# Kernel optimization log

Hardware: AMD Instinct MI355X
Metric: run time of the kernel (lower is better)

Reference implementation:

```python
import jax, jax.numpy as jnp
import numpy as np

N_NODES = 500_000
N_EDGES = 8_000_000
BN_EPS = 1e-5


def _graph_embed(src, dst, n, W_init, b_init, Wg, bg, Wt1, g1, b1, Wt2, g2, b2, Wd, bd):
    # init_graph: input is all-ones [n, 12] -> Linear(12->4); every row identical
    x_row = W_init.sum(0) + b_init                      # [4]
    h_row = jax.nn.sigmoid(x_row @ Wg + bg)             # node gating -> [7]
    h = jnp.broadcast_to(h_row, (n, h_row.shape[0]))    # [n, 7]

    # symmetric normalization, DGL TAGConv style
    deg = jnp.zeros((n,), jnp.float32).at[dst].add(1.0)
    norm = jnp.clip(deg, 1.0) ** -0.5                   # [n]

    def prop(x):  # x: [n, d] -> normalized adjacency propagation
        x = x * norm[:, None]
        agg = jnp.zeros_like(x).at[dst].add(x[src])
        return agg * norm[:, None]

    def tagconv(x, W):  # K=2: concat [h, Ah, A^2h] then linear (no bias)
        f1 = prop(x)
        f2 = prop(f1)
        return jnp.concatenate([x, f1, f2], axis=1) @ W

    def bn_relu(x, gamma, beta):  # BatchNorm1d training-mode (batch stats)
        m = x.mean(0)
        v = x.var(0)
        return jax.nn.relu((x - m) / jnp.sqrt(v + BN_EPS) * gamma + beta)

    h = bn_relu(tagconv(h, Wt1), g1, b1)
    h = bn_relu(tagconv(h, Wt2), g2, b2)
    h = h @ Wd + bd                                     # [n, 11]
    return h.mean(0)                                    # [11] graph embedding


def setup_inputs() -> dict:
    key = jax.random.key(0)
    ks = jax.random.split(key, 32)
    n, e = N_NODES, N_EDGES
    d = {
        "src1": jax.random.randint(ks[0], (e,), 0, n, dtype=jnp.int32),
        "dst1": jax.random.randint(ks[1], (e,), 0, n, dtype=jnp.int32),
        "src2": jax.random.randint(ks[2], (e,), 0, n, dtype=jnp.int32),
        "dst2": jax.random.randint(ks[3], (e,), 0, n, dtype=jnp.int32),
        "n_nodes": n,
    }
    def w(k, shape):
        return jax.random.normal(k, shape, jnp.float32) * 0.1
    # GraphEmbed params (node_emb=4, size_graph_emb=11, layers=(7,7), TAGConv K=2)
    d["W_init"] = w(ks[4], (12, 4)); d["b_init"] = w(ks[5], (4,))
    d["Wg"] = w(ks[6], (4, 7));      d["bg"] = w(ks[7], (7,))
    d["Wt1"] = w(ks[8], (21, 7))
    d["bn1_g"] = jnp.ones((7,), jnp.float32); d["bn1_b"] = jnp.zeros((7,), jnp.float32)
    d["Wt2"] = w(ks[9], (21, 7))
    d["bn2_g"] = jnp.ones((7,), jnp.float32); d["bn2_b"] = jnp.zeros((7,), jnp.float32)
    d["Wd"] = w(ks[10], (7, 11));    d["bd"] = w(ks[11], (11,))
    # GraphSimilarity params (embedding_space=11, layers=(7,7,7), 12 properties)
    d["Ws0"] = w(ks[12], (22, 7));   d["bs0"] = w(ks[13], (7,))
    d["Ws1"] = w(ks[14], (7, 7));    d["bs1"] = w(ks[15], (7,))
    d["Ws2"] = w(ks[16], (7, 7));    d["bs2"] = w(ks[17], (7,))
    d["Ws3"] = w(ks[18], (7, 7));    d["bs3"] = w(ks[19], (7,))
    d["Wsim"] = w(ks[20], (7, 12));  d["bsim"] = w(ks[21], (12,))
    return d


def reference(src1, dst1, src2, dst2, n_nodes,
              W_init, b_init, Wg, bg, Wt1, bn1_g, bn1_b, Wt2, bn2_g, bn2_b, Wd, bd,
              Ws0, bs0, Ws1, bs1, Ws2, bs2, Ws3, bs3, Wsim, bsim):
    emb = lambda s, t: _graph_embed(s, t, n_nodes, W_init, b_init, Wg, bg,
                                    Wt1, bn1_g, bn1_b, Wt2, bn2_g, bn2_b, Wd, bd)
    hg1 = emb(src1, dst1)
    hg2 = emb(src2, dst2)
    h = jnp.concatenate([hg1, hg2])[None, :]            # [1, 22]
    h = h @ Ws0 + bs0
    for W, b in ((Ws1, bs1), (Ws2, bs2), (Ws3, bs3)):
        h = jax.nn.relu(h @ W + b)
    logits = h @ Wsim + bsim                            # [1, 12]
    # sigmoid on locality logit and sigmoid on remaining diffs == elementwise sigmoid
    return jax.nn.sigmoid(logits)
```

## Files before the change

### kernel.cpp

```cpp
#include <hip/hip_runtime.h>
#include <hip/hip_bf16.h>
#include <math.h>

#define NNODES 500000
#define BN_EPS 1e-5f
#define BKT 512
#define NBKT ((NNODES + BKT - 1) / BKT)
#define EPB 16384

__device__ __forceinline__ int atomAddI(int* p, int v) {
    return __hip_atomic_fetch_add(p, v, __ATOMIC_RELAXED, __HIP_MEMORY_SCOPE_AGENT);
}
__device__ __forceinline__ void atomAddD(double* p, double v) {
    __hip_atomic_fetch_add(p, v, __ATOMIC_RELAXED, __HIP_MEMORY_SCOPE_AGENT);
}
__device__ __forceinline__ void ldsAddF(float* p, float v) {
    __hip_atomic_fetch_add(p, v, __ATOMIC_RELAXED, __HIP_MEMORY_SCOPE_WORKGROUP);
}

template<int CNT>
__device__ __forceinline__ void blk_reduce_atomic(double (&vals)[CNT], double* dst) {
    __shared__ double sh[CNT][4];
    int lane = threadIdx.x & 63, wid = threadIdx.x >> 6;
#pragma unroll
    for (int k = 0; k < CNT; ++k) {
        double v = vals[k];
#pragma unroll
        for (int o = 32; o; o >>= 1) v += __shfl_down(v, o);
        if (lane == 0) sh[k][wid] = v;
    }
    __syncthreads();
    if ((int)threadIdx.x < CNT) {
        double v = sh[threadIdx.x][0] + sh[threadIdx.x][1] + sh[threadIdx.x][2] + sh[threadIdx.x][3];
        atomAddD(dst + threadIdx.x, v);
    }
}

__global__ void k_t0(const float* __restrict__ Wi, const float* __restrict__ bi,
                     const float* __restrict__ Wg, const float* __restrict__ bg,
                     const float* __restrict__ Wt1, float* __restrict__ fs) {
    if (threadIdx.x || blockIdx.x) return;
    float xr[4];
    for (int j = 0; j < 4; ++j) {
        float s = bi[j];
        for (int k = 0; k < 12; ++k) s += Wi[k * 4 + j];
        xr[j] = s;
    }
    float hr[7];
    for (int j = 0; j < 7; ++j) {
        float s = bg[j];
        for (int k = 0; k < 4; ++k) s += xr[k] * Wg[k * 7 + j];
        hr[j] = 1.f / (1.f + expf(-s));
        fs[j] = hr[j];
    }
    for (int j = 0; j < 7; ++j) {
        float s0 = 0.f, s1 = 0.f, s2 = 0.f;
        for (int k = 0; k < 7; ++k) {
            s0 += hr[k] * Wt1[k * 7 + j];
            s1 += hr[k] * Wt1[(7 + k) * 7 + j];
            s2 += hr[k] * Wt1[(14 + k) * 7 + j];
        }
        fs[7 + j] = s0; fs[14 + j] = s1; fs[21 + j] = s2;
    }
}

__global__ void __launch_bounds__(256) k_bhist(const int* __restrict__ dst, int* __restrict__ gcnt, int E) {
    __shared__ int h[NBKT];
    for (int i = threadIdx.x; i < NBKT; i += 256) h[i] = 0;
    __syncthreads();
    int base = blockIdx.x * EPB;
#pragma unroll
    for (int k = 0; k < EPB / 1024; ++k) {
        int i4 = base + (k * 256 + threadIdx.x) * 4;
        if (i4 + 3 < E) {
            int4 d = *reinterpret_cast<const int4*>(dst + i4);
            atomicAdd(&h[d.x >> 9], 1); atomicAdd(&h[d.y >> 9], 1);
            atomicAdd(&h[d.z >> 9], 1); atomicAdd(&h[d.w >> 9], 1);
        } else {
            for (int i = i4; i < E && i < i4 + 4; ++i) atomicAdd(&h[dst[i] >> 9], 1);
        }
    }
    __syncthreads();
    for (int i = threadIdx.x; i < NBKT; i += 256)
        if (h[i]) atomAddI(gcnt + i, h[i]);
}

__global__ void __launch_bounds__(1024) k_bscan(const int* __restrict__ gcnt,
                                                int* __restrict__ bb, int* __restrict__ gcur) {
    __shared__ int sh[1024];
    int t = threadIdx.x;
    int v = (t < NBKT) ? gcnt[t] : 0;
    sh[t] = v; __syncthreads();
    for (int o = 1; o < 1024; o <<= 1) {
        int x = (t >= o) ? sh[t - o] : 0;
        __syncthreads();
        sh[t] += x;
        __syncthreads();
    }
    if (t < NBKT) { int ex = sh[t] - v; bb[t] = ex; gcur[t] = ex; }
    if (t == 0) bb[NBKT] = sh[1023];
}

__global__ void __launch_bounds__(256) k_bscat(const int* __restrict__ src, const int* __restrict__ dst,
                                               int* __restrict__ gcur, unsigned int* __restrict__ pairs, int E) {
    __shared__ int h[NBKT];
    for (int i = threadIdx.x; i < NBKT; i += 256) h[i] = 0;
    __syncthreads();
    int base = blockIdx.x * EPB;
#pragma unroll
    for (int k = 0; k < EPB / 1024; ++k) {
        int i4 = base + (k * 256 + threadIdx.x) * 4;
        if (i4 + 3 < E) {
            int4 d = *reinterpret_cast<const int4*>(dst + i4);
            atomicAdd(&h[d.x >> 9], 1); atomicAdd(&h[d.y >> 9], 1);
            atomicAdd(&h[d.z >> 9], 1); atomicAdd(&h[d.w >> 9], 1);
        } else {
            for (int i = i4; i < E && i < i4 + 4; ++i) atomicAdd(&h[dst[i] >> 9], 1);
        }
    }
    __syncthreads();
    for (int i = threadIdx.x; i < NBKT; i += 256) {
        int c = h[i];
        h[i] = c ? atomAddI(gcur + i, c) : 0;
    }
    __syncthreads();
#pragma unroll
    for (int k = 0; k < EPB / 1024; ++k) {
        int i4 = base + (k * 256 + threadIdx.x) * 4;
        if (i4 + 3 < E) {
            int4 s = *reinterpret_cast<const int4*>(src + i4);
            int4 d = *reinterpret_cast<const int4*>(dst + i4);
            int se[4] = {s.x, s.y, s.z, s.w};
            int de[4] = {d.x, d.y, d.z, d.w};
#pragma unroll
            for (int e = 0; e < 4; ++e) {
                int b = de[e] >> 9;
                int pos = atomicAdd(&h[b], 1);
                pairs[pos] = ((unsigned int)(de[e] & 511) << 19) | (unsigned int)se[e];
            }
        } else {
            for (int i = i4; i < E && i < i4 + 4; ++i) {
                int b = dst[i] >> 9;
                int pos = atomicAdd(&h[b], 1);
                pairs[pos] = ((unsigned int)(dst[i] & 511) << 19) | (unsigned int)src[i];
            }
        }
    }
}

__global__ void __launch_bounds__(256) k_deg(const unsigned int* __restrict__ pairs, const int* __restrict__ bb,
                                             float* __restrict__ nrm, float* __restrict__ sdeg, int n) {
    __shared__ int deg[BKT];
    int b = blockIdx.x, t = threadIdx.x;
    deg[t] = 0; deg[t + 256] = 0;
    __syncthreads();
    int lo = bb[b], hi = bb[b + 1];
    for (int k = lo + t; k < hi; k += 256) atomicAdd(&deg[pairs[k] >> 19], 1);
    __syncthreads();
#pragma unroll
    for (int j = 0; j < 2; ++j) {
        int dl = t + j * 256, node = b * BKT + dl;
        if (node < n) {
            float sd = sqrtf((float)(deg[dl] > 0 ? deg[dl] : 1));
            sdeg[node] = sd;
            nrm[node] = 1.f / sd;
        }
    }
}

__global__ void __launch_bounds__(256) k_s1(const unsigned int* __restrict__ pairs, const int* __restrict__ bb,
                                            const float* __restrict__ nrm, float* __restrict__ s1,
                                            float* __restrict__ s1n, int n) {
    __shared__ float acc[BKT];
    int b = blockIdx.x, t = threadIdx.x;
    acc[t] = 0.f; acc[t + 256] = 0.f;
    __syncthreads();
    int lo = bb[b], hi = bb[b + 1];
    for (int k = lo + t; k < hi; k += 256) {
        unsigned int v = pairs[k];
        ldsAddF(&acc[v >> 19], nrm[v & 0x7FFFF]);
    }
    __syncthreads();
#pragma unroll
    for (int j = 0; j < 2; ++j) {
        int dl = t + j * 256, node = b * BKT + dl;
        if (node < n) {
            float nn = nrm[node], v1 = acc[dl] * nn;
            s1[node] = v1; s1n[node] = v1 * nn;
        }
    }
}

__global__ void __launch_bounds__(256) k_s2(const unsigned int* __restrict__ pairs, const int* __restrict__ bb,
                                            const float* __restrict__ nrm, const float* __restrict__ s1,
                                            const float* __restrict__ s1n, float* __restrict__ s2,
                                            double* __restrict__ ds, int n) {
    __shared__ float acc[BKT];
    int b = blockIdx.x, t = threadIdx.x;
    acc[t] = 0.f; acc[t + 256] = 0.f;
    __syncthreads();
    int lo = bb[b], hi = bb[b + 1];
    for (int k = lo + t; k < hi; k += 256) {
        unsigned int v = pairs[k];
        ldsAddF(&acc[v >> 19], s1n[v & 0x7FFFF]);
    }
    __syncthreads();
    double m[5] = {0, 0, 0, 0, 0};
#pragma unroll
    for (int j = 0; j < 2; ++j) {
        int dl = t + j * 256, node = b * BKT + dl;
        if (node < n) {
            float nn = nrm[node], v2 = acc[dl] * nn;
            s2[node] = v2;
            float v1 = s1[node];
            m[0] += v1; m[1] += v2;
            m[2] += (double)v1 * (double)v1;
            m[3] += (double)v2 * (double)v2;
            m[4] += (double)v1 * (double)v2;
        }
    }
    blk_reduce_atomic<5>(m, ds);
}

__global__ void k_t1(const double* __restrict__ ds, const float* __restrict__ fs,
                     const float* __restrict__ g1, const float* __restrict__ b1, float* __restrict__ fsg) {
    if (threadIdx.x || blockIdx.x) return;
    const double inv_n = 1.0 / (double)NNODES;
    float mu1 = (float)(ds[0] * inv_n), mu2 = (float)(ds[1] * inv_n);
    float V11 = (float)(ds[2] * inv_n) - mu1 * mu1;
    float V22 = (float)(ds[3] * inv_n) - mu2 * mu2;
    float V12 = (float)(ds[4] * inv_n) - mu1 * mu2;
    for (int j = 0; j < 7; ++j) {
        float a1 = fs[14 + j], a2 = fs[21 + j];
        float var = a1 * a1 * V11 + a2 * a2 * V22 + 2.f * a1 * a2 * V12;
        float ig = (1.f / sqrtf(var + BN_EPS)) * g1[j];
        fsg[j]      = b1[j] - (mu1 * a1 + mu2 * a2) * ig;
        fsg[7 + j]  = a1 * ig;
        fsg[14 + j] = a2 * ig;
    }
}

__global__ void __launch_bounds__(256) k_h1n(const float* __restrict__ s1, const float* __restrict__ s2,
                                             const float* __restrict__ nrm, const float* __restrict__ fsg,
                                             float* __restrict__ h1n, int n) {
    int i = blockIdx.x * blockDim.x + threadIdx.x;
    if (i >= n) return;
    float S1 = s1[i], S2 = s2[i], Nn = nrm[i];
    float o[8];
#pragma unroll
    for (int j = 0; j < 7; ++j)
        o[j] = fmaxf(fsg[j] + S1 * fsg[7 + j] + S2 * fsg[14 + j], 0.f) * Nn;
    o[7] = 0.f;
    float4* q = reinterpret_cast<float4*>(h1n + (size_t)i * 8);
    q[0] = make_float4(o[0], o[1], o[2], o[3]);
    q[1] = make_float4(o[4], o[5], o[6], o[7]);
}

__global__ void __launch_bounds__(256) k_f1(const unsigned int* __restrict__ pairs, const int* __restrict__ bb,
                                            const float* __restrict__ nrm, const float* __restrict__ h1n,
                                            float* __restrict__ f1n, int n) {
    __shared__ float a[7][BKT];
    int b = blockIdx.x, t = threadIdx.x;
#pragma unroll
    for (int j = 0; j < 7; ++j) { a[j][t] = 0.f; a[j][t + 256] = 0.f; }
    __syncthreads();
    int lo = bb[b], hi = bb[b + 1];
    for (int k = lo + t; k < hi; k += 256) {
        unsigned int v = pairs[k];
        int s = v & 0x7FFFF, dl = v >> 19;
        const float4* p = reinterpret_cast<const float4*>(h1n + (size_t)s * 8);
        float4 x = p[0], y = p[1];
        ldsAddF(&a[0][dl], x.x); ldsAddF(&a[1][dl], x.y); ldsAddF(&a[2][dl], x.z);
        ldsAddF(&a[3][dl], x.w); ldsAddF(&a[4][dl], y.x); ldsAddF(&a[5][dl], y.y);
        ldsAddF(&a[6][dl], y.z);
    }
    __syncthreads();
#pragma unroll
    for (int j = 0; j < 2; ++j) {
        int dl = t + j * 256, node = b * BKT + dl;
        if (node < n) {
            float nn = nrm[node], sc = nn * nn;
            float4* q = reinterpret_cast<float4*>(f1n + (size_t)node * 8);
            q[0] = make_float4(a[0][dl] * sc, a[1][dl] * sc, a[2][dl] * sc, a[3][dl] * sc);
            q[1] = make_float4(a[4][dl] * sc, a[5][dl] * sc, a[6][dl] * sc, 0.f);
        }
    }
}

__global__ void __launch_bounds__(256) k_x2f(const unsigned int* __restrict__ pairs, const int* __restrict__ bb,
                                             const float* __restrict__ nrm, const float* __restrict__ sdeg,
                                             const float* __restrict__ s1, const float* __restrict__ s2,
                                             const float* __restrict__ fsg, const float* __restrict__ f1n,
                                             const float* __restrict__ Wt2, float* __restrict__ x2o,
                                             double* __restrict__ ds, int n) {
    __shared__ float a[7][BKT];
    __shared__ float w[147];
    int b = blockIdx.x, t = threadIdx.x;
    for (int k = t; k < 147; k += 256) w[k] = Wt2[k];
    float dc[21];
#pragma unroll
    for (int j = 0; j < 21; ++j) dc[j] = fsg[j];
#pragma unroll
    for (int j = 0; j < 7; ++j) { a[j][t] = 0.f; a[j][t + 256] = 0.f; }
    __syncthreads();
    int lo = bb[b], hi = bb[b + 1];
    for (int k = lo + t; k < hi; k += 256) {
        unsigned int v = pairs[k];
        int s = v & 0x7FFFF, dl = v >> 19;
        const float4* p = reinterpret_cast<const float4*>(f1n + (size_t)s * 8);
        float4 x = p[0], y = p[1];
        ldsAddF(&a[0][dl], x.x); ldsAddF(&a[1][dl], x.y); ldsAddF(&a[2][dl], x.z);
        ldsAddF(&a[3][dl], x.w); ldsAddF(&a[4][dl], y.x); ldsAddF(&a[5][dl], y.y);
        ldsAddF(&a[6][dl], y.z);
    }
    __syncthreads();
    double sx[7] = {0, 0, 0, 0, 0, 0, 0}, sq[7] = {0, 0, 0, 0, 0, 0, 0};
#pragma unroll
    for (int jj = 0; jj < 2; ++jj) {
        int dl = t + jj * 256, node = b * BKT + dl;
        if (node < n) {
            float S1 = s1[node], S2 = s2[node], Nn = nrm[node], rn = sdeg[node];
            float h1[7];
#pragma unroll
            for (int k = 0; k < 7; ++k) h1[k] = fmaxf(dc[k] + S1 * dc[7 + k] + S2 * dc[14 + k], 0.f);
            const float4* pf = reinterpret_cast<const float4*>(f1n + (size_t)node * 8);
            float4 fa = pf[0], fb = pf[1];
            float f1p[7] = {fa.x * rn, fa.y * rn, fa.z * rn, fa.w * rn, fb.x * rn, fb.y * rn, fb.z * rn};
            float f2p[7];
#pragma unroll
            for (int k = 0; k < 7; ++k) f2p[k] = a[k][dl] * Nn;
            float x2[8];
#pragma unroll
            for (int j = 0; j < 7; ++j) {
                float s = 0.f;
#pragma unroll
                for (int k = 0; k < 7; ++k)
                    s += h1[k] * w[k * 7 + j] + f1p[k] * w[(7 + k) * 7 + j] + f2p[k] * w[(14 + k) * 7 + j];
                x2[j] = s;
                sx[j] += s; sq[j] += (double)s * (double)s;
            }
            x2[7] = 0.f;
            float4* q = reinterpret_cast<float4*>(x2o + (size_t)node * 8);
            q[0] = make_float4(x2[0], x2[1], x2[2], x2[3]);
            q[1] = make_float4(x2[4], x2[5], x2[6], x2[7]);
        }
    }
    double acc[14];
#pragma unroll
    for (int j = 0; j < 7; ++j) { acc[j] = sx[j]; acc[7 + j] = sq[j]; }
    blk_reduce_atomic<14>(acc, ds + 5);
}

__global__ void k_t2(const double* __restrict__ ds, const float* __restrict__ g2,
                     const float* __restrict__ b2, float* __restrict__ fsg) {
    if (threadIdx.x || blockIdx.x) return;
    const double inv_n = 1.0 / (double)NNODES;
    for (int j = 0; j < 7; ++j) {
        float m = (float)(ds[5 + j] * inv_n);
        float v = (float)(ds[12 + j] * inv_n) - m * m;
        float ig = (1.f / sqrtf(v + BN_EPS)) * g2[j];
        fsg[21 + j] = b2[j] - m * ig;
        fsg[28 + j] = ig;
    }
}

__global__ void __launch_bounds__(256) k_h2sum(const float* __restrict__ x2o, const float* __restrict__ fsg,
                                               double* __restrict__ ds, int n) {
    float c0[7], c1[7];
#pragma unroll
    for (int j = 0; j < 7; ++j) { c0[j] = fsg[21 + j]; c1[j] = fsg[28 + j]; }
    double acc[7] = {0, 0, 0, 0, 0, 0, 0};
    for (int i = blockIdx.x * blockDim.x + threadIdx.x; i < n; i += gridDim.x * blockDim.x) {
        const float4* p = reinterpret_cast<const float4*>(x2o + (size_t)i * 8);
        float4 a = p[0], b = p[1];
        float x[7] = {a.x, a.y, a.z, a.w, b.x, b.y, b.z};
#pragma unroll
        for (int j = 0; j < 7; ++j) acc[j] += (double)fmaxf(x[j] * c1[j] + c0[j], 0.f);
    }
    blk_reduce_atomic<7>(acc, ds + 19);
}

__global__ void k_final(const double* __restrict__ ds, const float* __restrict__ Wd, const float* __restrict__ bd,
                        const float* __restrict__ Ws0, const float* __restrict__ bs0,
                        const float* __restrict__ Ws1, const float* __restrict__ bs1,
                        const float* __restrict__ Ws2, const float* __restrict__ bs2,
                        const float* __restrict__ Ws3, const float* __restrict__ bs3,
                        const float* __restrict__ Wsim, const float* __restrict__ bsim,
                        float* __restrict__ out) {
    if (threadIdx.x || blockIdx.x) return;
    const double inv_n = 1.0 / (double)NNODES;
    float v[22];
    for (int g = 0; g < 2; ++g) {
        float hm[7];
        for (int j = 0; j < 7; ++j) hm[j] = (float)(ds[g * 26 + 19 + j] * inv_n);
        for (int r = 0; r < 11; ++r) {
            float s = bd[r];
            for (int j = 0; j < 7; ++j) s += hm[j] * Wd[j * 11 + r];
            v[g * 11 + r] = s;
        }
    }
    float h[7], h2[7];
    for (int j = 0; j < 7; ++j) {
        float s = bs0[j];
        for (int k = 0; k < 22; ++k) s += v[k] * Ws0[k * 7 + j];
        h[j] = s;
    }
    const float* Ws[3] = {Ws1, Ws2, Ws3};
    const float* bs[3] = {bs1, bs2, bs3};
    for (int l = 0; l < 3; ++l) {
        for (int j = 0; j < 7; ++j) {
            float s = bs[l][j];
            for (int k = 0; k < 7; ++k) s += h[k] * Ws[l][k * 7 + j];
            h2[j] = fmaxf(s, 0.f);
        }
        for (int j = 0; j < 7; ++j) h[j] = h2[j];
    }
    for (int r = 0; r < 12; ++r) {
        float s = bsim[r];
        for (int j = 0; j < 7; ++j) s += h[j] * Wsim[j * 12 + r];
        out[r] = 1.f / (1.f + expf(-s));
    }
}

extern "C" void kernel_launch(void* const* d_in, const int* in_sizes, int n_in,
                              void* d_out, int out_size, void* d_ws, size_t ws_size,
                              hipStream_t stream) {
    const int E = in_sizes[0];
    const int n = NNODES;
    const int* src1 = (const int*)d_in[0];
    const int* dst1 = (const int*)d_in[1];
    const int* src2 = (const int*)d_in[2];
    const int* dst2 = (const int*)d_in[3];
    const float* W_init = (const float*)d_in[5];
    const float* b_init = (const float*)d_in[6];
    const float* Wg  = (const float*)d_in[7];
    const float* bg  = (const float*)d_in[8];
    const float* Wt1 = (const float*)d_in[9];
    const float* g1  = (const float*)d_in[10];
    const float* b1  = (const float*)d_in[11];
    const float* Wt2 = (const float*)d_in[12];
    const float* g2  = (const float*)d_in[13];
    const float* b2  = (const float*)d_in[14];
    const float* Wd  = (const float*)d_in[15];
    const float* bd  = (const float*)d_in[16];
    const float* Ws0 = (const float*)d_in[17];
    const float* bs0 = (const float*)d_in[18];
    const float* Ws1 = (const float*)d_in[19];
    const float* bs1 = (const float*)d_in[20];
    const float* Ws2 = (const float*)d_in[21];
    const float* bs2 = (const float*)d_in[22];
    const float* Ws3 = (const float*)d_in[23];
    const float* bs3 = (const float*)d_in[24];
    const float* Wsim = (const float*)d_in[25];
    const float* bsim = (const float*)d_in[26];

    float* F     = (float*)d_ws;
    float* norm  = F;
    float* sdeg  = F + (size_t)n;
    float* s1    = F + 2 * (size_t)n;
    float* s1n   = F + 3 * (size_t)n;
    float* s2    = F + 4 * (size_t)n;
    float* h1n   = F + 5 * (size_t)n;
    float* f1n   = F + 13 * (size_t)n;
    int*   gcnt  = (int*)(F + 21 * (size_t)n);
    int*   bb    = gcnt + NBKT;
    int*   gcur  = bb + NBKT + 1;
    unsigned int* pairs = (unsigned int*)(gcur + NBKT);
    float* fscal = (float*)(pairs + E);
    size_t dso = ((size_t)(fscal + 128 - F) + 1) & ~(size_t)1;
    double* dscal = (double*)(F + dso);

    const int EB  = (E + EPB - 1) / EPB;
    const int nbk = (n + 255) / 256;
    const int rbk = 1024;

    hipMemsetAsync(dscal, 0, 52 * sizeof(double), stream);
    k_t0<<<1, 1, 0, stream>>>(W_init, b_init, Wg, bg, Wt1, fscal);

    for (int g = 0; g < 2; ++g) {
        const int* src = g ? src2 : src1;
        const int* dst = g ? dst2 : dst1;
        float* fsg  = fscal + 28 + g * 35;
        double* dsg = dscal + g * 26;

        hipMemsetAsync(gcnt, 0, NBKT * sizeof(int), stream);
        k_bhist<<<EB, 256, 0, stream>>>(dst, gcnt, E);
        k_bscan<<<1, 1024, 0, stream>>>(gcnt, bb, gcur);
        k_bscat<<<EB, 256, 0, stream>>>(src, dst, gcur, pairs, E);

        k_deg<<<NBKT, 256, 0, stream>>>(pairs, bb, norm, sdeg, n);
        k_s1 <<<NBKT, 256, 0, stream>>>(pairs, bb, norm, s1, s1n, n);
        k_s2 <<<NBKT, 256, 0, stream>>>(pairs, bb, norm, s1, s1n, s2, dsg, n);
        k_t1<<<1, 1, 0, stream>>>(dsg, fscal, g1, b1, fsg);
        k_h1n<<<nbk, 256, 0, stream>>>(s1, s2, norm, fsg, h1n, n);
        k_f1 <<<NBKT, 256, 0, stream>>>(pairs, bb, norm, h1n, f1n, n);
        k_x2f<<<NBKT, 256, 0, stream>>>(pairs, bb, norm, sdeg, s1, s2, fsg, f1n, Wt2, h1n, dsg, n);
        k_t2<<<1, 1, 0, stream>>>(dsg, g2, b2, fsg);
        k_h2sum<<<rbk, 256, 0, stream>>>(h1n, fsg, dsg, n);
    }
    k_final<<<1, 1, 0, stream>>>(dscal, Wd, bd, Ws0, bs0, Ws1, bs1, Ws2, bs2, Ws3, bs3,
                                 Wsim, bsim, (float*)d_out);
}
```

Baseline: 2.053 ms.

## Fuse layer-1 activation into gather, pack node scalars, store f1 in fp16

Removes the separate k_h1n pass: k_f1 now rebuilds the layer-1 ReLU features on the fly from a packed per-node float4 (s1, s2, norm, sqrt-degree) instead of gathering a 32-byte h1n row. The f1 intermediate is stored as fp16 in 16-byte rows, which halves gather traffic in k_x2f. Bucket kernels move to 512 threads (one per node), and the edge loops are unrolled by two to keep more loads in flight. The cost is extra ALU work per edge in k_f1, a little fp16 precision loss on f1, and a new workspace layout.

```diff
diff --git a/kernel.cpp b/kernel.cpp
--- a/kernel.cpp
+++ b/kernel.cpp
@@ -1,5 +1,6 @@
 #include <hip/hip_runtime.h>
 #include <hip/hip_bf16.h>
+#include <hip/hip_fp16.h>
 #include <math.h>
 
 #define NNODES 500000
@@ -20,7 +21,7 @@
 
 template<int CNT>
 __device__ __forceinline__ void blk_reduce_atomic(double (&vals)[CNT], double* dst) {
-    __shared__ double sh[CNT][4];
+    __shared__ double sh[CNT][8];
     int lane = threadIdx.x & 63, wid = threadIdx.x >> 6;
 #pragma unroll
     for (int k = 0; k < CNT; ++k) {
@@ -31,7 +32,9 @@
     }
     __syncthreads();
     if ((int)threadIdx.x < CNT) {
-        double v = sh[threadIdx.x][0] + sh[threadIdx.x][1] + sh[threadIdx.x][2] + sh[threadIdx.x][3];
+        double v = 0.0;
+#pragma unroll
+        for (int w = 0; w < 8; ++w) v += sh[threadIdx.x][w];
         atomAddD(dst + threadIdx.x, v);
     }
 }
@@ -148,76 +151,83 @@
     }
 }
 
-__global__ void __launch_bounds__(256) k_deg(const unsigned int* __restrict__ pairs, const int* __restrict__ bb,
-                                             float* __restrict__ nrm, float* __restrict__ sdeg, int n) {
+__global__ void __launch_bounds__(512) k_deg(const unsigned int* __restrict__ pairs, const int* __restrict__ bb,
+                                             float* __restrict__ nrm, float* __restrict__ sc4, int n) {
     __shared__ int deg[BKT];
     int b = blockIdx.x, t = threadIdx.x;
-    deg[t] = 0; deg[t + 256] = 0;
+    deg[t] = 0;
     __syncthreads();
     int lo = bb[b], hi = bb[b + 1];
-    for (int k = lo + t; k < hi; k += 256) atomicAdd(&deg[pairs[k] >> 19], 1);
-    __syncthreads();
-#pragma unroll
-    for (int j = 0; j < 2; ++j) {
-        int dl = t + j * 256, node = b * BKT + dl;
-        if (node < n) {
-            float sd = sqrtf((float)(deg[dl] > 0 ? deg[dl] : 1));
-            sdeg[node] = sd;
-            nrm[node] = 1.f / sd;
-        }
-    }
-}
-
-__global__ void __launch_bounds__(256) k_s1(const unsigned int* __restrict__ pairs, const int* __restrict__ bb,
+    int k = lo + t;
+    for (; k + BKT < hi; k += 2 * BKT) {
+        unsigned int v1 = pairs[k], v2 = pairs[k + BKT];
+        atomicAdd(&deg[v1 >> 19], 1);
+        atomicAdd(&deg[v2 >> 19], 1);
+    }
+    if (k < hi) atomicAdd(&deg[pairs[k] >> 19], 1);
+    __syncthreads();
+    int node = b * BKT + t;
+    if (node < n) {
+        float sd = sqrtf((float)(deg[t] > 0 ? deg[t] : 1));
+        float nn = 1.f / sd;
+        nrm[node] = nn;
+        reinterpret_cast<float4*>(sc4)[node] = make_float4(0.f, 0.f, nn, sd);
+    }
+}
+
+__global__ void __launch_bounds__(512) k_s1(const unsigned int* __restrict__ pairs, const int* __restrict__ bb,
                                             const float* __restrict__ nrm, float* __restrict__ s1,
-                                            float* __restrict__ s1n, int n) {
+                                            float* __restrict__ s1n, float* __restrict__ sc4, int n) {
     __shared__ float acc[BKT];
     int b = blockIdx.x, t = threadIdx.x;
-    acc[t] = 0.f; acc[t + 256] = 0.f;
+    acc[t] = 0.f;
     __syncthreads();
     int lo = bb[b], hi = bb[b + 1];
-    for (int k = lo + t; k < hi; k += 256) {
-        unsigned int v = pairs[k];
-        ldsAddF(&acc[v >> 19], nrm[v & 0x7FFFF]);
-    }
-    __syncthreads();
-#pragma unroll
-    for (int j = 0; j < 2; ++j) {
-        int dl = t + j * 256, node = b * BKT + dl;
-        if (node < n) {
-            float nn = nrm[node], v1 = acc[dl] * nn;
-            s1[node] = v1; s1n[node] = v1 * nn;
-        }
-    }
-}
-
-__global__ void __launch_bounds__(256) k_s2(const unsigned int* __restrict__ pairs, const int* __restrict__ bb,
+    int k = lo + t;
+    for (; k + BKT < hi; k += 2 * BKT) {
+        unsigned int v1 = pairs[k], v2 = pairs[k + BKT];
+        float g1 = nrm[v1 & 0x7FFFF], g2 = nrm[v2 & 0x7FFFF];
+        ldsAddF(&acc[v1 >> 19], g1);
+        ldsAddF(&acc[v2 >> 19], g2);
+    }
+    if (k < hi) { unsigned int v = pairs[k]; ldsAddF(&acc[v >> 19], nrm[v & 0x7FFFF]); }
+    __syncthreads();
+    int node = b * BKT + t;
+    if (node < n) {
+        float nn = nrm[node], v1 = acc[t] * nn;
+        s1[node] = v1; s1n[node] = v1 * nn;
+        sc4[(size_t)node * 4 + 0] = v1;
+    }
+}
+
+__global__ void __launch_bounds__(512) k_s2(const unsigned int* __restrict__ pairs, const int* __restrict__ bb,
                                             const float* __restrict__ nrm, const float* __restrict__ s1,
-                                            const float* __restrict__ s1n, float* __restrict__ s2,
+                                            const float* __restrict__ s1n, float* __restrict__ sc4,
                                             double* __restrict__ ds, int n) {
     __shared__ float acc[BKT];
     int b = blockIdx.x, t = threadIdx.x;
-    acc[t] = 0.f; acc[t + 256] = 0.f;
+    acc[t] = 0.f;
     __syncthreads();
     int lo = bb[b], hi = bb[b + 1];
-    for (int k = lo + t; k < hi; k += 256) {
-        unsigned int v = pairs[k];
-        ldsAddF(&acc[v >> 19], s1n[v & 0x7FFFF]);
-    }
+    int k = lo + t;
+    for (; k + BKT < hi; k += 2 * BKT) {
+        unsigned int v1 = pairs[k], v2 = pairs[k + BKT];
+        float g1 = s1n[v1 & 0x7FFFF], g2 = s1n[v2 & 0x7FFFF];
+        ldsAddF(&acc[v1 >> 19], g1);
+        ldsAddF(&acc[v2 >> 19], g2);
+    }
+    if (k < hi) { unsigned int v = pairs[k]; ldsAddF(&acc[v >> 19], s1n[v & 0x7FFFF]); }
     __syncthreads();
     double m[5] = {0, 0, 0, 0, 0};
-#pragma unroll
-    for (int j = 0; j < 2; ++j) {
-        int dl = t + j * 256, node = b * BKT + dl;
-        if (node < n) {
-            float nn = nrm[node], v2 = acc[dl] * nn;
-            s2[node] = v2;
-            float v1 = s1[node];
-            m[0] += v1; m[1] += v2;
-            m[2] += (double)v1 * (double)v1;
-            m[3] += (double)v2 * (double)v2;
-            m[4] += (double)v1 * (double)v2;
-        }
+    int node = b * BKT + t;
+    if (node < n) {
+        float nn = nrm[node], v2 = acc[t] * nn;
+        sc4[(size_t)node * 4 + 1] = v2;
+        float v1 = s1[node];
+        m[0] += v1; m[1] += v2;
+        m[2] += (double)v1 * (double)v1;
+        m[3] += (double)v2 * (double)v2;
+        m[4] += (double)v1 * (double)v2;
     }
     blk_reduce_atomic<5>(m, ds);
 }
@@ -240,110 +250,138 @@
     }
 }
 
-__global__ void __launch_bounds__(256) k_h1n(const float* __restrict__ s1, const float* __restrict__ s2,
-                                             const float* __restrict__ nrm, const float* __restrict__ fsg,
-                                             float* __restrict__ h1n, int n) {
-    int i = blockIdx.x * blockDim.x + threadIdx.x;
-    if (i >= n) return;
-    float S1 = s1[i], S2 = s2[i], Nn = nrm[i];
-    float o[8];
-#pragma unroll
-    for (int j = 0; j < 7; ++j)
-        o[j] = fmaxf(fsg[j] + S1 * fsg[7 + j] + S2 * fsg[14 + j], 0.f) * Nn;
-    o[7] = 0.f;
-    float4* q = reinterpret_cast<float4*>(h1n + (size_t)i * 8);
-    q[0] = make_float4(o[0], o[1], o[2], o[3]);
-    q[1] = make_float4(o[4], o[5], o[6], o[7]);
-}
-
-__global__ void __launch_bounds__(256) k_f1(const unsigned int* __restrict__ pairs, const int* __restrict__ bb,
-                                            const float* __restrict__ nrm, const float* __restrict__ h1n,
-                                            float* __restrict__ f1n, int n) {
+__global__ void __launch_bounds__(512) k_f1(const unsigned int* __restrict__ pairs, const int* __restrict__ bb,
+                                            const float* __restrict__ nrm, const float* __restrict__ sc4,
+                                            const float* __restrict__ fsg, float* __restrict__ f1nh, int n) {
     __shared__ float a[7][BKT];
     int b = blockIdx.x, t = threadIdx.x;
-#pragma unroll
-    for (int j = 0; j < 7; ++j) { a[j][t] = 0.f; a[j][t + 256] = 0.f; }
+    float dc[21];
+#pragma unroll
+    for (int j = 0; j < 21; ++j) dc[j] = fsg[j];
+#pragma unroll
+    for (int j = 0; j < 7; ++j) a[j][t] = 0.f;
     __syncthreads();
     int lo = bb[b], hi = bb[b + 1];
-    for (int k = lo + t; k < hi; k += 256) {
+    int k = lo + t;
+    for (; k + BKT < hi; k += 2 * BKT) {
+        unsigned int v1 = pairs[k], v2 = pairs[k + BKT];
+        float4 r1 = reinterpret_cast<const float4*>(sc4)[v1 & 0x7FFFF];
+        float4 r2 = reinterpret_cast<const float4*>(sc4)[v2 & 0x7FFFF];
+        int d1 = v1 >> 19, d2 = v2 >> 19;
+#pragma unroll
+        for (int j = 0; j < 7; ++j) {
+            float h = fmaxf(dc[j] + r1.x * dc[7 + j] + r1.y * dc[14 + j], 0.f) * r1.z;
+            ldsAddF(&a[j][d1], h);
+        }
+#pragma unroll
+        for (int j = 0; j < 7; ++j) {
+            float h = fmaxf(dc[j] + r2.x * dc[7 + j] + r2.y * dc[14 + j], 0.f) * r2.z;
+            ldsAddF(&a[j][d2], h);
+        }
+    }
+    if (k < hi) {
         unsigned int v = pairs[k];
-        int s = v & 0x7FFFF, dl = v >> 19;
-        const float4* p = reinterpret_cast<const float4*>(h1n + (size_t)s * 8);
-        float4 x = p[0], y = p[1];
-        ldsAddF(&a[0][dl], x.x); ldsAddF(&a[1][dl], x.y); ldsAddF(&a[2][dl], x.z);
-        ldsAddF(&a[3][dl], x.w); ldsAddF(&a[4][dl], y.x); ldsAddF(&a[5][dl], y.y);
-        ldsAddF(&a[6][dl], y.z);
-    }
-    __syncthreads();
-#pragma unroll
-    for (int j = 0; j < 2; ++j) {
-        int dl = t + j * 256, node = b * BKT + dl;
-        if (node < n) {
-            float nn = nrm[node], sc = nn * nn;
-            float4* q = reinterpret_cast<float4*>(f1n + (size_t)node * 8);
-            q[0] = make_float4(a[0][dl] * sc, a[1][dl] * sc, a[2][dl] * sc, a[3][dl] * sc);
-            q[1] = make_float4(a[4][dl] * sc, a[5][dl] * sc, a[6][dl] * sc, 0.f);
-        }
-    }
-}
-
-__global__ void __launch_bounds__(256) k_x2f(const unsigned int* __restrict__ pairs, const int* __restrict__ bb,
-                                             const float* __restrict__ nrm, const float* __restrict__ sdeg,
-                                             const float* __restrict__ s1, const float* __restrict__ s2,
-                                             const float* __restrict__ fsg, const float* __restrict__ f1n,
-                                             const float* __restrict__ Wt2, float* __restrict__ x2o,
-                                             double* __restrict__ ds, int n) {
+        float4 r = reinterpret_cast<const float4*>(sc4)[v & 0x7FFFF];
+        int dl = v >> 19;
+#pragma unroll
+        for (int j = 0; j < 7; ++j) {
+            float h = fmaxf(dc[j] + r.x * dc[7 + j] + r.y * dc[14 + j], 0.f) * r.z;
+            ldsAddF(&a[j][dl], h);
+        }
+    }
+    __syncthreads();
+    int node = b * BKT + t;
+    if (node < n) {
+        float nn = nrm[node], sc = nn * nn;
+        __half2 hh[4];
+        hh[0] = __floats2half2_rn(a[0][t] * sc, a[1][t] * sc);
+        hh[1] = __floats2half2_rn(a[2][t] * sc, a[3][t] * sc);
+        hh[2] = __floats2half2_rn(a[4][t] * sc, a[5][t] * sc);
+        hh[3] = __floats2half2_rn(a[6][t] * sc, 0.f);
+        reinterpret_cast<float4*>(f1nh)[node] = *reinterpret_cast<float4*>(hh);
+    }
+}
+
+__global__ void __launch_bounds__(512) k_x2f(const unsigned int* __restrict__ pairs, const int* __restrict__ bb,
+                                             const float* __restrict__ sc4, const float* __restrict__ fsg,
+                                             const float* __restrict__ f1nh, const float* __restrict__ Wt2,
+                                             float* __restrict__ x2o, double* __restrict__ ds, int n) {
     __shared__ float a[7][BKT];
     __shared__ float w[147];
     int b = blockIdx.x, t = threadIdx.x;
-    for (int k = t; k < 147; k += 256) w[k] = Wt2[k];
+    for (int k = t; k < 147; k += 512) w[k] = Wt2[k];
     float dc[21];
 #pragma unroll
     for (int j = 0; j < 21; ++j) dc[j] = fsg[j];
 #pragma unroll
-    for (int j = 0; j < 7; ++j) { a[j][t] = 0.f; a[j][t + 256] = 0.f; }
+    for (int j = 0; j < 7; ++j) a[j][t] = 0.f;
     __syncthreads();
     int lo = bb[b], hi = bb[b + 1];
-    for (int k = lo + t; k < hi; k += 256) {
+    int k = lo + t;
+    for (; k + BKT < hi; k += 2 * BKT) {
+        unsigned int v1 = pairs[k], v2 = pairs[k + BKT];
+        float4 raw1 = reinterpret_cast<const float4*>(f1nh)[v1 & 0x7FFFF];
+        float4 raw2 = reinterpret_cast<const float4*>(f1nh)[v2 & 0x7FFFF];
+        int d1 = v1 >> 19, d2 = v2 >> 19;
+        {
+            const __half2* hp = reinterpret_cast<const __half2*>(&raw1);
+            float2 q0 = __half22float2(hp[0]), q1 = __half22float2(hp[1]);
+            float2 q2 = __half22float2(hp[2]), q3 = __half22float2(hp[3]);
+            ldsAddF(&a[0][d1], q0.x); ldsAddF(&a[1][d1], q0.y); ldsAddF(&a[2][d1], q1.x);
+            ldsAddF(&a[3][d1], q1.y); ldsAddF(&a[4][d1], q2.x); ldsAddF(&a[5][d1], q2.y);
+            ldsAddF(&a[6][d1], q3.x);
+        }
+        {
+            const __half2* hp = reinterpret_cast<const __half2*>(&raw2);
+            float2 q0 = __half22float2(hp[0]), q1 = __half22float2(hp[1]);
+            float2 q2 = __half22float2(hp[2]), q3 = __half22float2(hp[3]);
+            ldsAddF(&a[0][d2], q0.x); ldsAddF(&a[1][d2], q0.y); ldsAddF(&a[2][d2], q1.x);
+            ldsAddF(&a[3][d2], q1.y); ldsAddF(&a[4][d2], q2.x); ldsAddF(&a[5][d2], q2.y);
+            ldsAddF(&a[6][d2], q3.x);
+        }
+    }
+    if (k < hi) {
         unsigned int v = pairs[k];
-        int s = v & 0x7FFFF, dl = v >> 19;
-        const float4* p = reinterpret_cast<const float4*>(f1n + (size_t)s * 8);
-        float4 x = p[0], y = p[1];
-        ldsAddF(&a[0][dl], x.x); ldsAddF(&a[1][dl], x.y); ldsAddF(&a[2][dl], x.z);
-        ldsAddF(&a[3][dl], x.w); ldsAddF(&a[4][dl], y.x); ldsAddF(&a[5][dl], y.y);
-        ldsAddF(&a[6][dl], y.z);
+        float4 raw = reinterpret_cast<const float4*>(f1nh)[v & 0x7FFFF];
+        int dl = v >> 19;
+        const __half2* hp = reinterpret_cast<const __half2*>(&raw);
+        float2 q0 = __half22float2(hp[0]), q1 = __half22float2(hp[1]);
+        float2 q2 = __half22float2(hp[2]), q3 = __half22float2(hp[3]);
+        ldsAddF(&a[0][dl], q0.x); ldsAddF(&a[1][dl], q0.y); ldsAddF(&a[2][dl], q1.x);
+        ldsAddF(&a[3][dl], q1.y); ldsAddF(&a[4][dl], q2.x); ldsAddF(&a[5][dl], q2.y);
+        ldsAddF(&a[6][dl], q3.x);
     }
     __syncthreads();
     double sx[7] = {0, 0, 0, 0, 0, 0, 0}, sq[7] = {0, 0, 0, 0, 0, 0, 0};
-#pragma unroll
-    for (int jj = 0; jj < 2; ++jj) {
-        int dl = t + jj * 256, node = b * BKT + dl;
-        if (node < n) {
-            float S1 = s1[node], S2 = s2[node], Nn = nrm[node], rn = sdeg[node];
-            float h1[7];
-#pragma unroll
-            for (int k = 0; k < 7; ++k) h1[k] = fmaxf(dc[k] + S1 * dc[7 + k] + S2 * dc[14 + k], 0.f);
-            const float4* pf = reinterpret_cast<const float4*>(f1n + (size_t)node * 8);
-            float4 fa = pf[0], fb = pf[1];
-            float f1p[7] = {fa.x * rn, fa.y * rn, fa.z * rn, fa.w * rn, fb.x * rn, fb.y * rn, fb.z * rn};
-            float f2p[7];
-#pragma unroll
-            for (int k = 0; k < 7; ++k) f2p[k] = a[k][dl] * Nn;
-            float x2[8];
-#pragma unroll
-            for (int j = 0; j < 7; ++j) {
-                float s = 0.f;
-#pragma unroll
-                for (int k = 0; k < 7; ++k)
-                    s += h1[k] * w[k * 7 + j] + f1p[k] * w[(7 + k) * 7 + j] + f2p[k] * w[(14 + k) * 7 + j];
-                x2[j] = s;
-                sx[j] += s; sq[j] += (double)s * (double)s;
-            }
-            x2[7] = 0.f;
-            float4* q = reinterpret_cast<float4*>(x2o + (size_t)node * 8);
-            q[0] = make_float4(x2[0], x2[1], x2[2], x2[3]);
-            q[1] = make_float4(x2[4], x2[5], x2[6], x2[7]);
-        }
+    int node = b * BKT + t;
+    if (node < n) {
+        float4 s = reinterpret_cast<const float4*>(sc4)[node];
+        float S1 = s.x, S2 = s.y, Nn = s.z, rn = s.w;
+        float h1[7];
+#pragma unroll
+        for (int kk = 0; kk < 7; ++kk) h1[kk] = fmaxf(dc[kk] + S1 * dc[7 + kk] + S2 * dc[14 + kk], 0.f);
+        float4 raw = reinterpret_cast<const float4*>(f1nh)[node];
+        const __half2* hp = reinterpret_cast<const __half2*>(&raw);
+        float2 q0 = __half22float2(hp[0]), q1 = __half22float2(hp[1]);
+        float2 q2 = __half22float2(hp[2]), q3 = __half22float2(hp[3]);
+        float f1p[7] = {q0.x * rn, q0.y * rn, q1.x * rn, q1.y * rn, q2.x * rn, q2.y * rn, q3.x * rn};
+        float f2p[7];
+#pragma unroll
+        for (int kk = 0; kk < 7; ++kk) f2p[kk] = a[kk][t] * Nn;
+        float x2[8];
+#pragma unroll
+        for (int j = 0; j < 7; ++j) {
+            float sacc = 0.f;
+#pragma unroll
+            for (int kk = 0; kk < 7; ++kk)
+                sacc += h1[kk] * w[kk * 7 + j] + f1p[kk] * w[(7 + kk) * 7 + j] + f2p[kk] * w[(14 + kk) * 7 + j];
+            x2[j] = sacc;
+            sx[j] += sacc; sq[j] += (double)sacc * (double)sacc;
+        }
+        x2[7] = 0.f;
+        float4* q = reinterpret_cast<float4*>(x2o + (size_t)node * 8);
+        q[0] = make_float4(x2[0], x2[1], x2[2], x2[3]);
+        q[1] = make_float4(x2[4], x2[5], x2[6], x2[7]);
     }
     double acc[14];
 #pragma unroll
@@ -364,7 +402,7 @@
     }
 }
 
-__global__ void __launch_bounds__(256) k_h2sum(const float* __restrict__ x2o, const float* __restrict__ fsg,
+__global__ void __launch_bounds__(512) k_h2sum(const float* __restrict__ x2o, const float* __restrict__ fsg,
                                                double* __restrict__ ds, int n) {
     float c0[7], c1[7];
 #pragma unroll
@@ -454,25 +492,21 @@
     const float* Wsim = (const float*)d_in[25];
     const float* bsim = (const float*)d_in[26];
 
-    float* F     = (float*)d_ws;
-    float* norm  = F;
-    float* sdeg  = F + (size_t)n;
-    float* s1    = F + 2 * (size_t)n;
-    float* s1n   = F + 3 * (size_t)n;
-    float* s2    = F + 4 * (size_t)n;
-    float* h1n   = F + 5 * (size_t)n;
-    float* f1n   = F + 13 * (size_t)n;
-    int*   gcnt  = (int*)(F + 21 * (size_t)n);
-    int*   bb    = gcnt + NBKT;
-    int*   gcur  = bb + NBKT + 1;
+    double* dscal = (double*)d_ws;
+    float* fscal  = (float*)(dscal + 52);
+    float* F      = (float*)((char*)d_ws + 1024);
+    float* nrm  = F;
+    float* s1   = F + (size_t)n;
+    float* s1n  = F + 2 * (size_t)n;
+    float* sc4  = F + 3 * (size_t)n;
+    float* f1nh = F + 7 * (size_t)n;
+    float* x2o  = F + 11 * (size_t)n;
+    int*   gcnt = (int*)(F + 19 * (size_t)n);
+    int*   bb   = gcnt + NBKT;
+    int*   gcur = bb + NBKT + 1;
     unsigned int* pairs = (unsigned int*)(gcur + NBKT);
-    float* fscal = (float*)(pairs + E);
-    size_t dso = ((size_t)(fscal + 128 - F) + 1) & ~(size_t)1;
-    double* dscal = (double*)(F + dso);
-
-    const int EB  = (E + EPB - 1) / EPB;
-    const int nbk = (n + 255) / 256;
-    const int rbk = 1024;
+
+    const int EB = (E + EPB - 1) / EPB;
 
     hipMemsetAsync(dscal, 0, 52 * sizeof(double), stream);
     k_t0<<<1, 1, 0, stream>>>(W_init, b_init, Wg, bg, Wt1, fscal);
@@ -488,15 +522,14 @@
         k_bscan<<<1, 1024, 0, stream>>>(gcnt, bb, gcur);
         k_bscat<<<EB, 256, 0, stream>>>(src, dst, gcur, pairs, E);
 
-        k_deg<<<NBKT, 256, 0, stream>>>(pairs, bb, norm, sdeg, n);
-        k_s1 <<<NBKT, 256, 0, stream>>>(pairs, bb, norm, s1, s1n, n);
-        k_s2 <<<NBKT, 256, 0, stream>>>(pairs, bb, norm, s1, s1n, s2, dsg, n);
+        k_deg<<<NBKT, 512, 0, stream>>>(pairs, bb, nrm, sc4, n);
+        k_s1 <<<NBKT, 512, 0, stream>>>(pairs, bb, nrm, s1, s1n, sc4, n);
+        k_s2 <<<NBKT, 512, 0, stream>>>(pairs, bb, nrm, s1, s1n, sc4, dsg, n);
         k_t1<<<1, 1, 0, stream>>>(dsg, fscal, g1, b1, fsg);
-        k_h1n<<<nbk, 256, 0, stream>>>(s1, s2, norm, fsg, h1n, n);
-        k_f1 <<<NBKT, 256, 0, stream>>>(pairs, bb, norm, h1n, f1n, n);
-        k_x2f<<<NBKT, 256, 0, stream>>>(pairs, bb, norm, sdeg, s1, s2, fsg, f1n, Wt2, h1n, dsg, n);
+        k_f1 <<<NBKT, 512, 0, stream>>>(pairs, bb, nrm, sc4, fsg, f1nh, n);
+        k_x2f<<<NBKT, 512, 0, stream>>>(pairs, bb, sc4, fsg, f1nh, Wt2, x2o, dsg, n);
         k_t2<<<1, 1, 0, stream>>>(dsg, g2, b2, fsg);
-        k_h2sum<<<rbk, 256, 0, stream>>>(h1n, fsg, dsg, n);
+        k_h2sum<<<512, 512, 0, stream>>>(x2o, fsg, dsg, n);
     }
     k_final<<<1, 1, 0, stream>>>(dscal, Wd, bd, Ws0, bs0, Ws1, bs1, Ws2, bs2, Ws3, bs3,
                                  Wsim, bsim, (float*)d_out);
```

New measurement: 2.057 ms. Within noise of the previous version (+0.2%).
